# Kernel optimization log

Measured on AMD Instinct MI355X. Metric: run time of the kernel, lower is better.

## Reference

```python
import jax, jax.numpy as jnp
import numpy as np

N_INPUT = 1024
BATCH = 65536


def setup_inputs() -> dict:
    key = jax.random.key(0)
    kx, kA, kB = jax.random.split(key, 3)
    # average half must be strictly positive for pow(average, alpha)
    x = jax.random.uniform(kx, (BATCH, 2 * N_INPUT), dtype=jnp.float32,
                           minval=0.1, maxval=2.0)
    A = jax.random.normal(kA, (N_INPUT,), dtype=jnp.float32)
    B = jax.random.normal(kB, (N_INPUT, N_INPUT), dtype=jnp.float32)
    C = jnp.zeros((1,), dtype=jnp.float32)
    alpha = jnp.ones((N_INPUT,), dtype=jnp.float32)
    return {"x": x, "A": A, "B": B, "C": C, "alpha": alpha}


def reference(x, A, B, C, alpha):
    n = A.shape[0]
    average = x[:, :n]          # [batch, n]
    numbers = x[:, -n:]         # [batch, n]
    organelle = numbers * jnp.power(average, alpha)  # [batch, n]
    linear = organelle @ A                                   # [batch]
    quad = jnp.einsum('bi,ij,bj->b', organelle, B, organelle)  # batched quadratic form
    return linear + quad + C    # C broadcasts [1] -> [batch]
```

## Files before the change

kernel.cpp:

```cpp
#include <hip/hip_runtime.h>
#include <hip/hip_bf16.h>

typedef __bf16 bf16x8 __attribute__((ext_vector_type(8)));
typedef __bf16 bf16x4 __attribute__((ext_vector_type(4)));
typedef float  f32x4  __attribute__((ext_vector_type(4)));

#define N_IN 1024
#define BM   64
#define NTHR 512

__global__ void convB_kernel(const float* __restrict__ B, __bf16* __restrict__ Bb) {
    int i = blockIdx.x * blockDim.x + threadIdx.x;
    f32x4 v = ((const f32x4*)B)[i];
    bf16x4 o;
    o[0] = (__bf16)v[0]; o[1] = (__bf16)v[1]; o[2] = (__bf16)v[2]; o[3] = (__bf16)v[3];
    ((bf16x4*)Bb)[i] = o;
}

__global__ __launch_bounds__(256)
void pow_kernel(const float* __restrict__ x, const float* __restrict__ alpha,
                __bf16* __restrict__ O, int nvec) {
    for (int v = blockIdx.x * blockDim.x + threadIdx.x; v < nvec;
         v += gridDim.x * blockDim.x) {
        int row = v >> 7;
        int k   = (v & 127) << 3;
        const float* xr = x + (long)row * (2 * N_IN);
        f32x4 a0 = __builtin_nontemporal_load((const f32x4*)(xr + k));
        f32x4 a1 = __builtin_nontemporal_load((const f32x4*)(xr + k + 4));
        f32x4 n0 = __builtin_nontemporal_load((const f32x4*)(xr + N_IN + k));
        f32x4 n1 = __builtin_nontemporal_load((const f32x4*)(xr + N_IN + k + 4));
        f32x4 l0 = *(const f32x4*)(alpha + k);
        f32x4 l1 = *(const f32x4*)(alpha + k + 4);
        bf16x8 w;
        #pragma unroll
        for (int e = 0; e < 4; ++e) {
            w[e]     = (__bf16)(n0[e] * __expf(l0[e] * __logf(a0[e])));
            w[e + 4] = (__bf16)(n1[e] * __expf(l1[e] * __logf(a1[e])));
        }
        __builtin_nontemporal_store(w, (bf16x8*)(O + (long)row * N_IN + k));
    }
}

__global__ __launch_bounds__(NTHR, 2)
void qf_kernel(const __bf16* __restrict__ O, const __bf16* __restrict__ Bb,
               const float* __restrict__ A, const float* __restrict__ Cp,
               float* __restrict__ out) {
    __shared__ __align__(16) __bf16 o_panel[BM * N_IN];
    __shared__ float rowsum[8][BM];

    const int t    = threadIdx.x;
    const int wave = t >> 6;
    const int lane = t & 63;
    const int lrow = lane & 15;
    const int lgrp = lane >> 4;
    const long blk_row = (long)blockIdx.x * BM;
    const __bf16* Orow = O + blk_row * N_IN;

    {
        const int srow  = t >> 3;
        const int sk    = (t & 7) * 8;
        const int sw    = (srow & 7) << 3;
        #pragma unroll
        for (int c = 0; c < 16; ++c) {
            int k = c * 64 + sk;
            bf16x8 v = __builtin_nontemporal_load(
                (const bf16x8*)(Orow + (long)srow * N_IN + k));
            *(bf16x8*)&o_panel[srow * N_IN + (k ^ sw)] = v;
        }
    }
    __syncthreads();

    f32x4 acc[4][8];
    #pragma unroll
    for (int m = 0; m < 4; ++m)
        #pragma unroll
        for (int n = 0; n < 8; ++n)
            acc[m][n] = f32x4{0.f, 0.f, 0.f, 0.f};

    const __bf16* bbase = Bb + (long)(wave * 128 + lrow) * N_IN + lgrp * 8;
    auto loadB = [&](bf16x8* dst, int kc) {
        #pragma unroll
        for (int n = 0; n < 8; ++n)
            dst[n] = *(const bf16x8*)(bbase + (long)n * 16 * N_IN + kc * 32);
    };

    bf16x8 b0[8], b1[8];
    loadB(b0, 0);
    loadB(b1, 1);

    #pragma unroll 2
    for (int kc = 0; kc < 32; ++kc) {
        bf16x8* cur = (kc & 1) ? b1 : b0;
        const int kk = kc * 32 + lgrp * 8;
        bf16x8 afr[4];
        #pragma unroll
        for (int m = 0; m < 4; ++m) {
            int r = m * 16 + lrow;
            afr[m] = *(const bf16x8*)&o_panel[r * N_IN + (kk ^ ((r & 7) << 3))];
        }
        #pragma unroll
        for (int m = 0; m < 4; ++m)
            #pragma unroll
            for (int n = 0; n < 8; ++n)
                acc[m][n] = __builtin_amdgcn_mfma_f32_16x16x32_bf16(
                    afr[m], cur[n], acc[m][n], 0, 0, 0);
        if (kc + 2 < 32) loadB(cur, kc + 2);
    }

    float rp[16];
    #pragma unroll
    for (int i = 0; i < 16; ++i) rp[i] = 0.f;
    #pragma unroll
    for (int n = 0; n < 8; ++n) {
        const int i = wave * 128 + n * 16 + lrow;
        const float Ai = A[i];
        #pragma unroll
        for (int m = 0; m < 4; ++m)
            #pragma unroll
            for (int j = 0; j < 4; ++j) {
                const int r = m * 16 + lgrp * 4 + j;
                float ov = (float)o_panel[r * N_IN + ((i & ~7) ^ ((r & 7) << 3)) + (i & 7)];
                rp[m * 4 + j] += (acc[m][n][j] + Ai) * ov;
            }
    }
    #pragma unroll
    for (int d = 1; d < 16; d <<= 1)
        #pragma unroll
        for (int i = 0; i < 16; ++i)
            rp[i] += __shfl_xor(rp[i], d);
    if (lrow == 0) {
        #pragma unroll
        for (int m = 0; m < 4; ++m)
            #pragma unroll
            for (int j = 0; j < 4; ++j)
                rowsum[wave][m * 16 + lgrp * 4 + j] = rp[m * 4 + j];
    }
    __syncthreads();
    if (t < BM) {
        float s = Cp[0];
        #pragma unroll
        for (int w = 0; w < 8; ++w) s += rowsum[w][t];
        out[blk_row + t] = s;
    }
}

template<bool USEBF>
__global__ __launch_bounds__(NTHR, 2)
void fused_kernel(const float* __restrict__ x, const float* __restrict__ A,
                  const float* __restrict__ Bf, const __bf16* __restrict__ Bb,
                  const float* __restrict__ Cp, const float* __restrict__ alpha,
                  float* __restrict__ out) {
    __shared__ __align__(16) __bf16 o_panel[BM * N_IN];
    __shared__ float rowsum[8][BM];
    const int t = threadIdx.x, wave = t >> 6, lane = t & 63;
    const int lrow = lane & 15, lgrp = lane >> 4;
    const long blk_row = (long)blockIdx.x * BM;
    const int srow = t >> 3, skoff = (t & 7) * 4;
    const float* xrow = x + (blk_row + srow) * (2 * N_IN);
    #pragma unroll
    for (int c = 0; c < 8; ++c) {
        int k = c * 32 + skoff;
        f32x4 sa = *(const f32x4*)(xrow + k);
        f32x4 sn = *(const f32x4*)(xrow + N_IN + k);
        f32x4 sal = *(const f32x4*)(alpha + k);
        bf16x4 w4;
        #pragma unroll
        for (int e = 0; e < 4; ++e)
            w4[e] = (__bf16)(sn[e] * __expf(sal[e] * __logf(sa[e])));
        *(bf16x4*)&o_panel[srow * N_IN + ((k & ~7) ^ ((srow & 7) << 3)) + (k & 7)] = w4;
    }
    __syncthreads();
    f32x4 acc[2][4][4];
    #pragma unroll
    for (int h = 0; h < 2; ++h)
        #pragma unroll
        for (int m = 0; m < 4; ++m)
            #pragma unroll
            for (int n = 0; n < 4; ++n)
                acc[h][m][n] = f32x4{0.f, 0.f, 0.f, 0.f};
    #pragma unroll 1
    for (int q = 0; q < 4; ++q) {
        #pragma unroll
        for (int kq = 0; kq < 8; ++kq) {
            const int kc = q * 8 + kq;
            const bool staging = (q < 3);
            const int kk = kc * 32 + lgrp * 8;
            f32x4 sa, sn, sal;
            if (staging) {
                int k = (kc + 8) * 32 + skoff;
                sa = *(const f32x4*)(xrow + k);
                sn = *(const f32x4*)(xrow + N_IN + k);
                sal = *(const f32x4*)(alpha + k);
            }
            bf16x8 afr[4];
            #pragma unroll
            for (int m = 0; m < 4; ++m) {
                int r = m * 16 + lrow;
                afr[m] = *(const bf16x8*)&o_panel[r * N_IN + (kk ^ ((r & 7) << 3))];
            }
            bf16x8 bfr[2][4];
            #pragma unroll
            for (int h = 0; h < 2; ++h)
                #pragma unroll
                for (int n = 0; n < 4; ++n) {
                    int i = h * 512 + wave * 64 + n * 16 + lrow;
                    if constexpr (USEBF) {
                        bfr[h][n] = *(const bf16x8*)&Bb[(long)i * N_IN + kk];
                    } else {
                        const float* p = Bf + (long)i * N_IN + kk;
                        f32x4 lo = *(const f32x4*)p;
                        f32x4 hi = *(const f32x4*)(p + 4);
                        #pragma unroll
                        for (int e = 0; e < 4; ++e) {
                            bfr[h][n][e] = (__bf16)lo[e];
                            bfr[h][n][e + 4] = (__bf16)hi[e];
                        }
                    }
                }
            #pragma unroll
            for (int h = 0; h < 2; ++h)
                #pragma unroll
                for (int m = 0; m < 4; ++m)
                    #pragma unroll
                    for (int n = 0; n < 4; ++n)
                        acc[h][m][n] = __builtin_amdgcn_mfma_f32_16x16x32_bf16(
                            afr[m], bfr[h][n], acc[h][m][n], 0, 0, 0);
            if (staging) {
                int k = (kc + 8) * 32 + skoff;
                bf16x4 w4;
                #pragma unroll
                for (int e = 0; e < 4; ++e)
                    w4[e] = (__bf16)(sn[e] * __expf(sal[e] * __logf(sa[e])));
                *(bf16x4*)&o_panel[srow * N_IN + ((k & ~7) ^ ((srow & 7) << 3)) + (k & 7)] = w4;
            }
        }
        __syncthreads();
    }
    float rowpart[16];
    #pragma unroll
    for (int i = 0; i < 16; ++i) rowpart[i] = 0.f;
    #pragma unroll
    for (int h = 0; h < 2; ++h)
        #pragma unroll
        for (int n = 0; n < 4; ++n) {
            int i = h * 512 + wave * 64 + n * 16 + lrow;
            float Ai = A[i];
            #pragma unroll
            for (int m = 0; m < 4; ++m)
                #pragma unroll
                for (int j = 0; j < 4; ++j) {
                    int r = m * 16 + lgrp * 4 + j;
                    float y = acc[h][m][n][j] + Ai;
                    float ov = (float)o_panel[r * N_IN + ((i & ~7) ^ ((r & 7) << 3)) + (i & 7)];
                    rowpart[m * 4 + j] += y * ov;
                }
        }
    #pragma unroll
    for (int d = 1; d < 16; d <<= 1)
        #pragma unroll
        for (int i = 0; i < 16; ++i)
            rowpart[i] += __shfl_xor(rowpart[i], d);
    if (lrow == 0) {
        #pragma unroll
        for (int m = 0; m < 4; ++m)
            #pragma unroll
            for (int j = 0; j < 4; ++j)
                rowsum[wave][m * 16 + lgrp * 4 + j] = rowpart[m * 4 + j];
    }
    __syncthreads();
    if (t < BM) {
        float s = Cp[0];
        #pragma unroll
        for (int w = 0; w < 8; ++w) s += rowsum[w][t];
        out[blk_row + t] = s;
    }
}

extern "C" void kernel_launch(void* const* d_in, const int* in_sizes, int n_in,
                              void* d_out, int out_size, void* d_ws, size_t ws_size,
                              hipStream_t stream) {
    const float* x     = (const float*)d_in[0];
    const float* A     = (const float*)d_in[1];
    const float* B     = (const float*)d_in[2];
    const float* C     = (const float*)d_in[3];
    const float* alpha = (const float*)d_in[4];
    float* out = (float*)d_out;

    const int batch = in_sizes[0] / (2 * N_IN);
    const size_t bb_bytes = (size_t)N_IN * N_IN * 2;
    const size_t o_bytes  = (size_t)batch * N_IN * 2;

    if (ws_size >= bb_bytes + o_bytes) {
        __bf16* Bb = (__bf16*)d_ws;
        __bf16* O  = (__bf16*)((char*)d_ws + bb_bytes);
        convB_kernel<<<(N_IN * N_IN / 4) / 256, 256, 0, stream>>>(B, Bb);
        int nvec = batch * (N_IN / 8);
        pow_kernel<<<2048, 256, 0, stream>>>(x, alpha, O, nvec);
        qf_kernel<<<batch / BM, NTHR, 0, stream>>>(O, Bb, A, C, out);
    } else if (ws_size >= bb_bytes) {
        __bf16* Bb = (__bf16*)d_ws;
        convB_kernel<<<(N_IN * N_IN / 4) / 256, 256, 0, stream>>>(B, Bb);
        fused_kernel<true><<<batch / BM, NTHR, 0, stream>>>(x, A, nullptr, Bb, C, alpha, out);
    } else {
        fused_kernel<false><<<batch / BM, NTHR, 0, stream>>>(x, A, B, nullptr, C, alpha, out);
    }
}
```

Baseline: 392.9 us.

## Retile quadratic-form GEMM into 256x256 blocks with double-buffered K tiles and split reduction

The qf kernel now gives each block a 256-row by 256-column output tile instead of a 64-row by full-1024-column strip. The A operand is streamed through a double-buffered 256x64 LDS tile using raw barriers, so each B fragment is reused across more rows. Four column blocks write per-row partial sums to a workspace, and a new reduce kernel adds them together with C. The epilogue now reads O from global memory instead of LDS. The scheme needs more workspace and an extra launch, and the larger accumulator count (32 f32x4 per lane) may raise register pressure.

```diff
diff --git a/kernel.cpp b/kernel.cpp
--- a/kernel.cpp
+++ b/kernel.cpp
@@ -6,8 +6,13 @@
 typedef float  f32x4  __attribute__((ext_vector_type(4)));
 
 #define N_IN 1024
-#define BM   64
 #define NTHR 512
+
+#define RAW_BARRIER() do {                                      \
+    asm volatile("s_waitcnt lgkmcnt(0)" ::: "memory");          \
+    __builtin_amdgcn_s_barrier();                               \
+    asm volatile("" ::: "memory");                              \
+} while (0)
 
 __global__ void convB_kernel(const float* __restrict__ B, __bf16* __restrict__ Bb) {
     int i = blockIdx.x * blockDim.x + threadIdx.x;
@@ -43,105 +48,139 @@
 
 __global__ __launch_bounds__(NTHR, 2)
 void qf_kernel(const __bf16* __restrict__ O, const __bf16* __restrict__ Bb,
-               const float* __restrict__ A, const float* __restrict__ Cp,
-               float* __restrict__ out) {
-    __shared__ __align__(16) __bf16 o_panel[BM * N_IN];
-    __shared__ float rowsum[8][BM];
-
-    const int t    = threadIdx.x;
-    const int wave = t >> 6;
-    const int lane = t & 63;
+               const float* __restrict__ A, float* __restrict__ partial, int batch) {
+    __shared__ __align__(16) __bf16 atile[2][256 * 64];
+    __shared__ float rowsum[4][256];
+
+    const int t0   = threadIdx.x;
+    const int wave = t0 >> 6;
+    const int lane = t0 & 63;
     const int lrow = lane & 15;
     const int lgrp = lane >> 4;
-    const long blk_row = (long)blockIdx.x * BM;
-    const __bf16* Orow = O + blk_row * N_IN;
-
-    {
-        const int srow  = t >> 3;
-        const int sk    = (t & 7) * 8;
-        const int sw    = (srow & 7) << 3;
-        #pragma unroll
-        for (int c = 0; c < 16; ++c) {
-            int k = c * 64 + sk;
-            bf16x8 v = __builtin_nontemporal_load(
-                (const bf16x8*)(Orow + (long)srow * N_IN + k));
-            *(bf16x8*)&o_panel[srow * N_IN + (k ^ sw)] = v;
-        }
-    }
-    __syncthreads();
-
-    f32x4 acc[4][8];
-    #pragma unroll
-    for (int m = 0; m < 4; ++m)
-        #pragma unroll
-        for (int n = 0; n < 8; ++n)
+    const int wm   = wave >> 2;
+    const int wn   = wave & 3;
+    const int rowpanel = blockIdx.x & 255;
+    const int colblk   = blockIdx.x >> 8;
+    const long blk_row = (long)rowpanel * 256;
+    const int colbase  = colblk * 256 + wn * 64;
+
+    const int srow = t0 >> 1;
+    const int g0   = (t0 & 1) * 4;
+    const int s7   = srow & 7;
+    const __bf16* asrc = O + (blk_row + srow) * N_IN;
+
+    const __bf16* bbase = Bb + (long)(colbase + lrow) * N_IN + lgrp * 8;
+
+    f32x4 acc[8][4];
+    #pragma unroll
+    for (int m = 0; m < 8; ++m)
+        #pragma unroll
+        for (int n = 0; n < 4; ++n)
             acc[m][n] = f32x4{0.f, 0.f, 0.f, 0.f};
 
-    const __bf16* bbase = Bb + (long)(wave * 128 + lrow) * N_IN + lgrp * 8;
+    bf16x8 b0[4], b1[4];
     auto loadB = [&](bf16x8* dst, int kc) {
         #pragma unroll
-        for (int n = 0; n < 8; ++n)
+        for (int n = 0; n < 4; ++n)
             dst[n] = *(const bf16x8*)(bbase + (long)n * 16 * N_IN + kc * 32);
     };
 
-    bf16x8 b0[8], b1[8];
+    {
+        bf16x8 s[4];
+        #pragma unroll
+        for (int u = 0; u < 4; ++u)
+            s[u] = *(const bf16x8*)(asrc + (g0 + u) * 8);
+        #pragma unroll
+        for (int u = 0; u < 4; ++u)
+            *(bf16x8*)&atile[0][srow * 64 + (((g0 + u) ^ s7) << 3)] = s[u];
+    }
     loadB(b0, 0);
     loadB(b1, 1);
-
-    #pragma unroll 2
-    for (int kc = 0; kc < 32; ++kc) {
-        bf16x8* cur = (kc & 1) ? b1 : b0;
-        const int kk = kc * 32 + lgrp * 8;
-        bf16x8 afr[4];
-        #pragma unroll
-        for (int m = 0; m < 4; ++m) {
-            int r = m * 16 + lrow;
-            afr[m] = *(const bf16x8*)&o_panel[r * N_IN + (kk ^ ((r & 7) << 3))];
+    RAW_BARRIER();
+
+    #pragma unroll 1
+    for (int t = 0; t < 16; ++t) {
+        const int ts = (t + 1 < 16) ? t + 1 : 15;
+        bf16x8 s[4];
+        #pragma unroll
+        for (int u = 0; u < 4; ++u)
+            s[u] = *(const bf16x8*)(asrc + ts * 64 + (g0 + u) * 8);
+
+        #pragma unroll
+        for (int kq = 0; kq < 2; ++kq) {
+            const int kc = 2 * t + kq;
+            bf16x8* cur = kq ? b1 : b0;
+            bf16x8 afr[8];
+            #pragma unroll
+            for (int m = 0; m < 8; ++m) {
+                const int r  = wm * 128 + m * 16 + lrow;
+                const int gg = kq * 4 + lgrp;
+                afr[m] = *(const bf16x8*)&atile[t & 1][r * 64 + ((gg ^ (r & 7)) << 3)];
+            }
+            #pragma unroll
+            for (int m = 0; m < 8; ++m)
+                #pragma unroll
+                for (int n = 0; n < 4; ++n)
+                    acc[m][n] = __builtin_amdgcn_mfma_f32_16x16x32_bf16(
+                        afr[m], cur[n], acc[m][n], 0, 0, 0);
+            if (kc + 2 < 32) loadB(cur, kc + 2);
         }
-        #pragma unroll
-        for (int m = 0; m < 4; ++m)
-            #pragma unroll
-            for (int n = 0; n < 8; ++n)
-                acc[m][n] = __builtin_amdgcn_mfma_f32_16x16x32_bf16(
-                    afr[m], cur[n], acc[m][n], 0, 0, 0);
-        if (kc + 2 < 32) loadB(cur, kc + 2);
-    }
-
-    float rp[16];
-    #pragma unroll
-    for (int i = 0; i < 16; ++i) rp[i] = 0.f;
-    #pragma unroll
-    for (int n = 0; n < 8; ++n) {
-        const int i = wave * 128 + n * 16 + lrow;
+
+        #pragma unroll
+        for (int u = 0; u < 4; ++u)
+            *(bf16x8*)&atile[(t + 1) & 1][srow * 64 + (((g0 + u) ^ s7) << 3)] = s[u];
+        RAW_BARRIER();
+    }
+
+    float rp[32];
+    #pragma unroll
+    for (int i = 0; i < 32; ++i) rp[i] = 0.f;
+    #pragma unroll
+    for (int n = 0; n < 4; ++n) {
+        const int i = colbase + n * 16 + lrow;
         const float Ai = A[i];
         #pragma unroll
-        for (int m = 0; m < 4; ++m)
+        for (int m = 0; m < 8; ++m)
             #pragma unroll
             for (int j = 0; j < 4; ++j) {
-                const int r = m * 16 + lgrp * 4 + j;
-                float ov = (float)o_panel[r * N_IN + ((i & ~7) ^ ((r & 7) << 3)) + (i & 7)];
+                const long r = blk_row + wm * 128 + m * 16 + lgrp * 4 + j;
+                float ov = (float)O[r * N_IN + i];
                 rp[m * 4 + j] += (acc[m][n][j] + Ai) * ov;
             }
     }
     #pragma unroll
     for (int d = 1; d < 16; d <<= 1)
         #pragma unroll
-        for (int i = 0; i < 16; ++i)
+        for (int i = 0; i < 32; ++i)
             rp[i] += __shfl_xor(rp[i], d);
     if (lrow == 0) {
         #pragma unroll
-        for (int m = 0; m < 4; ++m)
+        for (int m = 0; m < 8; ++m)
             #pragma unroll
             for (int j = 0; j < 4; ++j)
-                rowsum[wave][m * 16 + lgrp * 4 + j] = rp[m * 4 + j];
+                rowsum[wn][wm * 128 + m * 16 + lgrp * 4 + j] = rp[m * 4 + j];
     }
     __syncthreads();
-    if (t < BM) {
-        float s = Cp[0];
-        #pragma unroll
-        for (int w = 0; w < 8; ++w) s += rowsum[w][t];
-        out[blk_row + t] = s;
-    }
+    if (t0 < 256) {
+        float s = rowsum[0][t0] + rowsum[1][t0] + rowsum[2][t0] + rowsum[3][t0];
+        partial[(long)colblk * batch + blk_row + t0] = s;
+    }
+}
+
+__global__ __launch_bounds__(256)
+void reduce_kernel(const float* __restrict__ partial, const float* __restrict__ Cp,
+                   float* __restrict__ out, int batch) {
+    int b = (blockIdx.x * 256 + threadIdx.x) * 4;
+    if (b >= batch) return;
+    f32x4 s = *(const f32x4*)(partial + b);
+    #pragma unroll
+    for (int c = 1; c < 4; ++c) {
+        f32x4 p = *(const f32x4*)(partial + (long)c * batch + b);
+        s[0] += p[0]; s[1] += p[1]; s[2] += p[2]; s[3] += p[3];
+    }
+    float C = Cp[0];
+    f32x4 o; o[0] = s[0] + C; o[1] = s[1] + C; o[2] = s[2] + C; o[3] = s[3] + C;
+    *(f32x4*)(out + b) = o;
 }
 
 template<bool USEBF>
@@ -150,11 +189,11 @@
                   const float* __restrict__ Bf, const __bf16* __restrict__ Bb,
                   const float* __restrict__ Cp, const float* __restrict__ alpha,
                   float* __restrict__ out) {
-    __shared__ __align__(16) __bf16 o_panel[BM * N_IN];
-    __shared__ float rowsum[8][BM];
+    __shared__ __align__(16) __bf16 o_panel[64 * N_IN];
+    __shared__ float rowsum[8][64];
     const int t = threadIdx.x, wave = t >> 6, lane = t & 63;
     const int lrow = lane & 15, lgrp = lane >> 4;
-    const long blk_row = (long)blockIdx.x * BM;
+    const long blk_row = (long)blockIdx.x * 64;
     const int srow = t >> 3, skoff = (t & 7) * 4;
     const float* xrow = x + (blk_row + srow) * (2 * N_IN);
     #pragma unroll
@@ -268,7 +307,7 @@
                 rowsum[wave][m * 16 + lgrp * 4 + j] = rowpart[m * 4 + j];
     }
     __syncthreads();
-    if (t < BM) {
+    if (t < 64) {
         float s = Cp[0];
         #pragma unroll
         for (int w = 0; w < 8; ++w) s += rowsum[w][t];
@@ -289,19 +328,21 @@
     const int batch = in_sizes[0] / (2 * N_IN);
     const size_t bb_bytes = (size_t)N_IN * N_IN * 2;
     const size_t o_bytes  = (size_t)batch * N_IN * 2;
-
-    if (ws_size >= bb_bytes + o_bytes) {
-        __bf16* Bb = (__bf16*)d_ws;
-        __bf16* O  = (__bf16*)((char*)d_ws + bb_bytes);
+    const size_t p_bytes  = (size_t)4 * batch * 4;
+
+    if (ws_size >= bb_bytes + o_bytes + p_bytes) {
+        __bf16* Bb     = (__bf16*)d_ws;
+        __bf16* O      = (__bf16*)((char*)d_ws + bb_bytes);
+        float*  part   = (float*)((char*)d_ws + bb_bytes + o_bytes);
         convB_kernel<<<(N_IN * N_IN / 4) / 256, 256, 0, stream>>>(B, Bb);
-        int nvec = batch * (N_IN / 8);
-        pow_kernel<<<2048, 256, 0, stream>>>(x, alpha, O, nvec);
-        qf_kernel<<<batch / BM, NTHR, 0, stream>>>(O, Bb, A, C, out);
+        pow_kernel<<<2048, 256, 0, stream>>>(x, alpha, O, batch * (N_IN / 8));
+        qf_kernel<<<(batch / 256) * 4, NTHR, 0, stream>>>(O, Bb, A, part, batch);
+        reduce_kernel<<<(batch / 4 + 255) / 256, 256, 0, stream>>>(part, C, out, batch);
     } else if (ws_size >= bb_bytes) {
         __bf16* Bb = (__bf16*)d_ws;
         convB_kernel<<<(N_IN * N_IN / 4) / 256, 256, 0, stream>>>(B, Bb);
-        fused_kernel<true><<<batch / BM, NTHR, 0, stream>>>(x, A, nullptr, Bb, C, alpha, out);
+        fused_kernel<true><<<batch / 64, NTHR, 0, stream>>>(x, A, nullptr, Bb, C, alpha, out);
     } else {
-        fused_kernel<false><<<batch / BM, NTHR, 0, stream>>>(x, A, B, nullptr, C, alpha, out);
-    }
-}
+        fused_kernel<false><<<batch / 64, NTHR, 0, stream>>>(x, A, B, nullptr, C, alpha, out);
+    }
+}
```

Result: slower. 466.5 us (+18.7%).
